# Optimization experiments

Measured on AMD Instinct MI355X. Metric: run time of the kernel, lower is better.

Reference implementation:

```python
import jax, jax.numpy as jnp
import numpy as np

B, S, D, H, F = 8, 1024, 768, 12, 3072
DH = D // H
C_QUAD = 5.0
LN_EPS = 1e-5


def layer_norm(x, g, b):
    mu = jnp.mean(x, axis=-1, keepdims=True)
    var = jnp.mean(jnp.square(x - mu), axis=-1, keepdims=True)
    return (x - mu) * jax.lax.rsqrt(var + LN_EPS) * g + b


def setup_inputs() -> dict:
    key = jax.random.key(0)
    ks = jax.random.split(key, 8)
    s_in = 1.0 / np.sqrt(D)
    s_ff = 1.0 / np.sqrt(F)
    return {
        "x": jax.random.normal(ks[0], (B, S, D), jnp.float32),
        "wqkv": jax.random.normal(ks[1], (D, 3 * D), jnp.float32) * s_in,
        "bqkv": jnp.zeros((3 * D,), jnp.float32),
        "wo": jax.random.normal(ks[2], (D, D), jnp.float32) * s_in,
        "bo": jnp.zeros((D,), jnp.float32),
        "ln1_g": jnp.ones((D,), jnp.float32),
        "ln1_b": jnp.zeros((D,), jnp.float32),
        "w1": jax.random.normal(ks[3], (D, F), jnp.float32) * s_in,
        "b1": jnp.zeros((F,), jnp.float32),
        "w2": jax.random.normal(ks[4], (F, D), jnp.float32) * s_ff,
        "b2": jnp.zeros((D,), jnp.float32),
        "ln2_g": jnp.ones((D,), jnp.float32),
        "ln2_b": jnp.zeros((D,), jnp.float32),
    }


def quad2(scores):
    # Quad2 custom 'softmax': (s + c)^2 normalized by row sum
    s2 = jnp.square(scores + C_QUAD)
    return s2 / jnp.sum(s2, axis=-1, keepdims=True)


def reference(x, wqkv, bqkv, wo, bo, ln1_g, ln1_b, w1, b1, w2, b2, ln2_g, ln2_b):
    # --- pre-norm multi-head attention with Quad2 score normalization ---
    h = layer_norm(x, ln1_g, ln1_b)
    qkv = h @ wqkv + bqkv                              # [B,S,3D]
    q, k, v = jnp.split(qkv, 3, axis=-1)
    q = q.reshape(B, S, H, DH).transpose(0, 2, 1, 3)   # [B,H,S,Dh]
    k = k.reshape(B, S, H, DH).transpose(0, 2, 1, 3)
    v = v.reshape(B, S, H, DH).transpose(0, 2, 1, 3)
    scale = 1.0 / np.sqrt(DH)
    scores = jnp.einsum("bhqd,bhkd->bhqk", q, k) * scale
    attn = quad2(scores)                               # [B,H,S,S]
    ctx = jnp.einsum("bhqk,bhkd->bhqd", attn, v)
    ctx = ctx.transpose(0, 2, 1, 3).reshape(B, S, D)
    x = x + ctx @ wo + bo
    # --- pre-norm FFN ---
    h = layer_norm(x, ln2_g, ln2_b)
    h = jax.nn.gelu(h @ w1 + b1)
    x = x + h @ w2 + b2
    return x
```

## Files before the change

kernel.cpp:

```cpp
#include <hip/hip_runtime.h>
#include <hip/hip_bf16.h>

constexpr int B_ = 8;
constexpr int S_ = 1024;
constexpr int D_ = 768;
constexpr int H_ = 12;
constexpr int F_ = 3072;
constexpr int DH_ = 64;
constexpr int M_ = B_ * S_;
constexpr int PSZ = B_ * S_ * D_;

typedef __bf16 bf16x8 __attribute__((ext_vector_type(8)));
typedef float f32x4 __attribute__((ext_vector_type(4)));
typedef short s16x8 __attribute__((ext_vector_type(8)));
typedef short s16x4 __attribute__((ext_vector_type(4)));

__device__ __forceinline__ void gload_lds16(const __bf16* g, __bf16* l) {
    __builtin_amdgcn_global_load_lds(
        (const __attribute__((address_space(1))) void*)g,
        (__attribute__((address_space(3))) void*)l,
        16, 0, 0);
}

__device__ __forceinline__ float fast_gelu(float x) {
    float z = 0.7978845608028654f * (x + 0.044715f * x * x * x);
    z = fminf(fmaxf(z, -15.0f), 15.0f);
    float e = __builtin_amdgcn_exp2f(2.8853900817779268f * z);
    float th = (e - 1.0f) / (e + 1.0f);
    return 0.5f * x * (1.0f + th);
}

__global__ __launch_bounds__(256) void transpose_cvt(const float* __restrict__ in,
                                                     __bf16* __restrict__ out,
                                                     int K, int N) {
    __shared__ float t[32][33];
    int tx = threadIdx.x, ty = threadIdx.y;
    int n0 = blockIdx.x * 32, k0 = blockIdx.y * 32;
#pragma unroll
    for (int i = 0; i < 4; ++i)
        t[ty + i * 8][tx] = in[(size_t)(k0 + ty + i * 8) * N + n0 + tx];
    __syncthreads();
#pragma unroll
    for (int i = 0; i < 4; ++i)
        out[(size_t)(n0 + ty + i * 8) * K + k0 + tx] = (__bf16)t[tx][ty + i * 8];
}

__global__ __launch_bounds__(256) void ln_kernel(const float* __restrict__ x,
                                                 const float* __restrict__ g,
                                                 const float* __restrict__ bb,
                                                 __bf16* __restrict__ out) {
    int row = blockIdx.x;
    const float* xr = x + (size_t)row * D_;
    int tid = threadIdx.x;
    float v[3];
    float s = 0.f, s2 = 0.f;
#pragma unroll
    for (int j = 0; j < 3; ++j) {
        v[j] = xr[tid + j * 256];
        s += v[j];
        s2 += v[j] * v[j];
    }
#pragma unroll
    for (int o = 32; o >= 1; o >>= 1) {
        s += __shfl_xor(s, o, 64);
        s2 += __shfl_xor(s2, o, 64);
    }
    __shared__ float red[8];
    int wid = tid >> 6, lane = tid & 63;
    if (lane == 0) { red[wid] = s; red[4 + wid] = s2; }
    __syncthreads();
    s = red[0] + red[1] + red[2] + red[3];
    s2 = red[4] + red[5] + red[6] + red[7];
    float mu = s * (1.0f / D_);
    float var = s2 * (1.0f / D_) - mu * mu;
    float rs = rsqrtf(var + 1e-5f);
    __bf16* orow = out + (size_t)row * D_;
#pragma unroll
    for (int j = 0; j < 3; ++j) {
        int i = tid + j * 256;
        orow[i] = (__bf16)((v[j] - mu) * rs * g[i] + bb[i]);
    }
}

template <int EPI>
__global__ __launch_bounds__(256) void gemm4(const __bf16* __restrict__ A,
                                             const __bf16* __restrict__ Bt,
                                             const float* __restrict__ bias,
                                             const float* __restrict__ res,
                                             float* __restrict__ outf,
                                             __bf16* __restrict__ outb,
                                             int M, int N, int K) {
    constexpr int BK = 64;
    __shared__ __bf16 lds[2][256 * BK];

    const int tid = threadIdx.x;
    const int lane = tid & 63, wid = tid >> 6;
    const int wm = wid >> 1, wn = wid & 1;
    const int bm = blockIdx.y * 128, bn = blockIdx.x * 128;
    const int l15 = lane & 15, l4 = lane >> 4;
    f32x4 acc[4][4] = {};

    const int r8 = tid >> 3;
    const int swc = ((tid & 7) ^ (r8 & 7)) * 8;
    const __bf16* ga = A + (size_t)(bm + r8) * K + swc;
    const __bf16* gb = Bt + (size_t)(bn + r8) * K + swc;
    const int NT = K / BK;

    auto stage = [&](int t, int s) {
        const int kt = t * BK;
        __bf16* base = &lds[s][0] + tid * 8;
#pragma unroll
        for (int j = 0; j < 4; ++j)
            gload_lds16(ga + kt + (size_t)j * 32 * K, base + j * 2048);
#pragma unroll
        for (int j = 0; j < 4; ++j)
            gload_lds16(gb + kt + (size_t)j * 32 * K, base + 8192 + j * 2048);
    };

    auto compute = [&](int s) {
        const __bf16* sA = &lds[s][0];
        const __bf16* sB = &lds[s][0] + 8192;
        const int swr = (l15 & 7) * 8;
        bf16x8 a[4][2], b[4][2];
#pragma unroll
        for (int mf = 0; mf < 4; ++mf) {
            int row = wm * 64 + mf * 16 + l15;
#pragma unroll
            for (int ks = 0; ks < 2; ++ks)
                a[mf][ks] = *(const bf16x8*)&sA[row * 64 + ((ks * 32 + l4 * 8) ^ swr)];
        }
#pragma unroll
        for (int nf = 0; nf < 4; ++nf) {
            int row = wn * 64 + nf * 16 + l15;
#pragma unroll
            for (int ks = 0; ks < 2; ++ks)
                b[nf][ks] = *(const bf16x8*)&sB[row * 64 + ((ks * 32 + l4 * 8) ^ swr)];
        }
        __builtin_amdgcn_s_setprio(1);
#pragma unroll
        for (int ks = 0; ks < 2; ++ks)
#pragma unroll
            for (int mf = 0; mf < 4; ++mf)
#pragma unroll
                for (int nf = 0; nf < 4; ++nf)
                    acc[mf][nf] = __builtin_amdgcn_mfma_f32_16x16x32_bf16(
                        a[mf][ks], b[nf][ks], acc[mf][nf], 0, 0, 0);
        __builtin_amdgcn_s_setprio(0);
    };

    stage(0, 0);
    for (int t = 0; t < NT; ++t) {
        if (t + 1 < NT) {
            stage(t + 1, (t + 1) & 1);
            asm volatile("s_waitcnt vmcnt(8)" ::: "memory");
        } else {
            asm volatile("s_waitcnt vmcnt(0)" ::: "memory");
        }
        asm volatile("s_barrier" ::: "memory");
        compute(t & 1);
        asm volatile("s_barrier" ::: "memory");
    }

#pragma unroll
    for (int mf = 0; mf < 4; ++mf) {
#pragma unroll
        for (int nf = 0; nf < 4; ++nf) {
#pragma unroll
            for (int r = 0; r < 4; ++r) {
                int m = bm + wm * 64 + mf * 16 + l4 * 4 + r;
                int n = bn + wn * 64 + nf * 16 + l15;
                float val = acc[mf][nf][r] + bias[n];
                if constexpr (EPI == 0) {
                    int part = n / 768;
                    int n7 = n - part * 768;
                    int head = n7 >> 6, dh = n7 & 63;
                    int bI = m >> 10, sI = m & 1023;
                    outb[(size_t)part * PSZ +
                         (((size_t)bI * H_ + head) * S_ + sI) * DH_ + dh] = (__bf16)val;
                } else if constexpr (EPI == 1) {
                    outf[(size_t)m * N + n] = val + res[(size_t)m * N + n];
                } else {
                    outb[(size_t)m * N + n] = (__bf16)fast_gelu(val);
                }
            }
        }
    }
}

__global__ __launch_bounds__(256) void attn_kernel(const __bf16* __restrict__ qg,
                                                   const __bf16* __restrict__ kg,
                                                   const __bf16* __restrict__ vg,
                                                   __bf16* __restrict__ ctx) {
    __shared__ __bf16 Ks[64][72];
    __shared__ __bf16 Vt[64][72];
    __shared__ __bf16 Pw[4][32][72];
    __shared__ float den_l[4][32];
    int tid = threadIdx.x, lane = tid & 63, wid = tid >> 6;
    int l15 = lane & 15, l4 = lane >> 4;
    int bh = blockIdx.x >> 3, qt = blockIdx.x & 7;
    int q0 = qt * 128;
    const __bf16* qbase = qg + (size_t)bh * S_ * DH_;
    const __bf16* kbase = kg + (size_t)bh * S_ * DH_;
    const __bf16* vbase = vg + (size_t)bh * S_ * DH_;

    int wq0 = q0 + wid * 32;
    bf16x8 qf[2][2];
#pragma unroll
    for (int qi = 0; qi < 2; ++qi)
#pragma unroll
        for (int ks = 0; ks < 2; ++ks)
            qf[qi][ks] = *(const bf16x8*)(qbase + (size_t)(wq0 + qi * 16 + l15) * DH_ +
                                          ks * 32 + l4 * 8);

    f32x4 oacc[2][4] = {};
    float den[2] = {0.f, 0.f};
    const float scale = 0.125f;

    for (int k0 = 0; k0 < S_; k0 += 64) {
        {
            int key = tid >> 2, dc = (tid & 3) * 16;
            *(s16x8*)&Ks[key][dc] =
                *(const s16x8*)(kbase + (size_t)(k0 + key) * DH_ + dc);
            *(s16x8*)&Ks[key][dc + 8] =
                *(const s16x8*)(kbase + (size_t)(k0 + key) * DH_ + dc + 8);
            int vkey = tid & 63, dg = (tid >> 6) * 16;
            s16x8 v0 = *(const s16x8*)(vbase + (size_t)(k0 + vkey) * DH_ + dg);
            s16x8 v1 = *(const s16x8*)(vbase + (size_t)(k0 + vkey) * DH_ + dg + 8);
#pragma unroll
            for (int e = 0; e < 8; ++e) {
                Vt[dg + e][vkey] = ((const __bf16*)&v0)[e];
                Vt[dg + 8 + e][vkey] = ((const __bf16*)&v1)[e];
            }
        }
        __syncthreads();

        bf16x8 kf[4][2];
#pragma unroll
        for (int kfi = 0; kfi < 4; ++kfi)
#pragma unroll
            for (int ks = 0; ks < 2; ++ks)
                kf[kfi][ks] = *(const bf16x8*)&Ks[kfi * 16 + l15][ks * 32 + l4 * 8];

#pragma unroll
        for (int qi = 0; qi < 2; ++qi) {
#pragma unroll
            for (int kfi = 0; kfi < 4; ++kfi) {
                f32x4 sa = {};
                sa = __builtin_amdgcn_mfma_f32_16x16x32_bf16(kf[kfi][0], qf[qi][0], sa, 0, 0, 0);
                sa = __builtin_amdgcn_mfma_f32_16x16x32_bf16(kf[kfi][1], qf[qi][1], sa, 0, 0, 0);
                __bf16 pk[4];
#pragma unroll
                for (int r = 0; r < 4; ++r) {
                    float p = sa[r] * scale + 5.0f;
                    p = p * p;
                    den[qi] += p;
                    pk[r] = (__bf16)p;
                }
                *(s16x4*)&Pw[wid][qi * 16 + l15][kfi * 16 + l4 * 4] =
                    *(const s16x4*)pk;
            }
        }

#pragma unroll
        for (int mf = 0; mf < 2; ++mf) {
#pragma unroll
            for (int ks = 0; ks < 2; ++ks) {
                bf16x8 pa = *(const bf16x8*)&Pw[wid][mf * 16 + l15][ks * 32 + l4 * 8];
#pragma unroll
                for (int nf = 0; nf < 4; ++nf) {
                    bf16x8 vb = *(const bf16x8*)&Vt[nf * 16 + l15][ks * 32 + l4 * 8];
                    oacc[mf][nf] = __builtin_amdgcn_mfma_f32_16x16x32_bf16(
                        pa, vb, oacc[mf][nf], 0, 0, 0);
                }
            }
        }
        __syncthreads();
    }

#pragma unroll
    for (int qi = 0; qi < 2; ++qi) {
        den[qi] += __shfl_xor(den[qi], 16, 64);
        den[qi] += __shfl_xor(den[qi], 32, 64);
    }
    if (lane < 16) {
        den_l[wid][lane] = den[0];
        den_l[wid][16 + lane] = den[1];
    }
    __syncthreads();

    int b_ = bh / H_, h_ = bh - b_ * H_;
#pragma unroll
    for (int mf = 0; mf < 2; ++mf)
#pragma unroll
        for (int nf = 0; nf < 4; ++nf)
#pragma unroll
            for (int r = 0; r < 4; ++r) {
                int qrow = mf * 16 + l4 * 4 + r;
                int dcol = nf * 16 + l15;
                float val = oacc[mf][nf][r] / den_l[wid][qrow];
                int sI = q0 + wid * 32 + qrow;
                ctx[((size_t)b_ * S_ + sI) * D_ + h_ * DH_ + dcol] = (__bf16)val;
            }
}

extern "C" void kernel_launch(void* const* d_in, const int* in_sizes, int n_in,
                              void* d_out, int out_size, void* d_ws, size_t ws_size,
                              hipStream_t stream) {
    const float* x    = (const float*)d_in[0];
    const float* wqkv = (const float*)d_in[1];
    const float* bqkv = (const float*)d_in[2];
    const float* wo   = (const float*)d_in[3];
    const float* bo   = (const float*)d_in[4];
    const float* ln1g = (const float*)d_in[5];
    const float* ln1b = (const float*)d_in[6];
    const float* w1   = (const float*)d_in[7];
    const float* b1   = (const float*)d_in[8];
    const float* w2   = (const float*)d_in[9];
    const float* b2   = (const float*)d_in[10];
    const float* ln2g = (const float*)d_in[11];
    const float* ln2b = (const float*)d_in[12];
    float* out = (float*)d_out;

    char* ws = (char*)d_ws;
    size_t off = 0;
    auto alloc = [&](size_t bytes) {
        void* p = ws + off;
        off += (bytes + 255) & ~(size_t)255;
        return p;
    };
    __bf16* wqkvT = (__bf16*)alloc((size_t)(3 * D_) * D_ * 2);
    __bf16* woT   = (__bf16*)alloc((size_t)D_ * D_ * 2);
    __bf16* w1T   = (__bf16*)alloc((size_t)F_ * D_ * 2);
    __bf16* w2T   = (__bf16*)alloc((size_t)D_ * F_ * 2);
    float*  X2    = (float*)alloc((size_t)M_ * D_ * 4);
    __bf16* Hb    = (__bf16*)alloc((size_t)M_ * D_ * 2);
    __bf16* Q3    = (__bf16*)alloc((size_t)4 * PSZ * 2);
    __bf16* Kb = Q3 + (size_t)PSZ;
    __bf16* Vb = Q3 + (size_t)2 * PSZ;
    __bf16* Cx = Q3 + (size_t)3 * PSZ;

    transpose_cvt<<<dim3((3 * D_) / 32, D_ / 32), dim3(32, 8), 0, stream>>>(wqkv, wqkvT, D_, 3 * D_);
    transpose_cvt<<<dim3(D_ / 32, D_ / 32), dim3(32, 8), 0, stream>>>(wo, woT, D_, D_);
    transpose_cvt<<<dim3(F_ / 32, D_ / 32), dim3(32, 8), 0, stream>>>(w1, w1T, D_, F_);
    transpose_cvt<<<dim3(D_ / 32, F_ / 32), dim3(32, 8), 0, stream>>>(w2, w2T, F_, D_);

    ln_kernel<<<M_, 256, 0, stream>>>(x, ln1g, ln1b, Hb);
    gemm4<0><<<dim3((3 * D_) / 128, M_ / 128), 256, 0, stream>>>(
        Hb, wqkvT, bqkv, nullptr, nullptr, Q3, M_, 3 * D_, D_);
    attn_kernel<<<B_ * H_ * (S_ / 128), 256, 0, stream>>>(Q3, Kb, Vb, Cx);
    gemm4<1><<<dim3(D_ / 128, M_ / 128), 256, 0, stream>>>(
        Cx, woT, bo, x, X2, nullptr, M_, D_, D_);
    ln_kernel<<<M_, 256, 0, stream>>>(X2, ln2g, ln2b, Hb);
    gemm4<2><<<dim3(F_ / 128, M_ / 128), 256, 0, stream>>>(
        Hb, w1T, b1, nullptr, nullptr, Q3, M_, F_, D_);
    gemm4<1><<<dim3(D_ / 128, M_ / 128), 256, 0, stream>>>(
        Q3, w2T, b2, X2, out, nullptr, M_, D_, F_);
    (void)in_sizes; (void)n_in; (void)out_size; (void)ws_size;
}
```

Baseline: 255.3 us.

## Remap GEMM workgroups across XCDs, restructure K loop and epilogues, use fast reciprocals

Several independent changes land together. GEMM workgroup IDs are permuted so consecutive tiles spread across the 8 XCDs for better L2 locality. The LDS reads are now followed by an lgkmcnt wait and a barrier before the MFMAs, which releases the LDS buffer earlier. The QKV epilogue hoists address arithmetic out of the inner loop. GELU becomes a sigmoid form using rcp, and the attention normalization multiplies by rcp instead of dividing. These trade small precision differences and an extra barrier for less ALU work, with some risk that the XCD remap ordering is not exact when the grid is not divisible by 8.

```diff
diff --git a/kernel.cpp b/kernel.cpp
--- a/kernel.cpp
+++ b/kernel.cpp
@@ -23,11 +23,10 @@
 }
 
 __device__ __forceinline__ float fast_gelu(float x) {
-    float z = 0.7978845608028654f * (x + 0.044715f * x * x * x);
-    z = fminf(fmaxf(z, -15.0f), 15.0f);
-    float e = __builtin_amdgcn_exp2f(2.8853900817779268f * z);
-    float th = (e - 1.0f) / (e + 1.0f);
-    return 0.5f * x * (1.0f + th);
+    float x3 = x * x * x;
+    float z = 0.7978845608028654f * x + 0.035677408136300125f * x3;
+    float e = __builtin_amdgcn_exp2f(-2.8853900817779268f * z);
+    return x * __builtin_amdgcn_rcpf(1.0f + e);
 }
 
 __global__ __launch_bounds__(256) void transpose_cvt(const float* __restrict__ in,
@@ -96,7 +95,11 @@
     const int tid = threadIdx.x;
     const int lane = tid & 63, wid = tid >> 6;
     const int wm = wid >> 1, wn = wid & 1;
-    const int bm = blockIdx.y * 128, bn = blockIdx.x * 128;
+    const int gx = gridDim.x;
+    const int nwg = gx * gridDim.y;
+    int flat = blockIdx.y * gx + blockIdx.x;
+    flat = (flat & 7) * (nwg >> 3) + (flat >> 3);
+    const int bm = (flat / gx) * 128, bn = (flat % gx) * 128;
     const int l15 = lane & 15, l4 = lane >> 4;
     f32x4 acc[4][4] = {};
 
@@ -115,37 +118,6 @@
 #pragma unroll
         for (int j = 0; j < 4; ++j)
             gload_lds16(gb + kt + (size_t)j * 32 * K, base + 8192 + j * 2048);
-    };
-
-    auto compute = [&](int s) {
-        const __bf16* sA = &lds[s][0];
-        const __bf16* sB = &lds[s][0] + 8192;
-        const int swr = (l15 & 7) * 8;
-        bf16x8 a[4][2], b[4][2];
-#pragma unroll
-        for (int mf = 0; mf < 4; ++mf) {
-            int row = wm * 64 + mf * 16 + l15;
-#pragma unroll
-            for (int ks = 0; ks < 2; ++ks)
-                a[mf][ks] = *(const bf16x8*)&sA[row * 64 + ((ks * 32 + l4 * 8) ^ swr)];
-        }
-#pragma unroll
-        for (int nf = 0; nf < 4; ++nf) {
-            int row = wn * 64 + nf * 16 + l15;
-#pragma unroll
-            for (int ks = 0; ks < 2; ++ks)
-                b[nf][ks] = *(const bf16x8*)&sB[row * 64 + ((ks * 32 + l4 * 8) ^ swr)];
-        }
-        __builtin_amdgcn_s_setprio(1);
-#pragma unroll
-        for (int ks = 0; ks < 2; ++ks)
-#pragma unroll
-            for (int mf = 0; mf < 4; ++mf)
-#pragma unroll
-                for (int nf = 0; nf < 4; ++nf)
-                    acc[mf][nf] = __builtin_amdgcn_mfma_f32_16x16x32_bf16(
-                        a[mf][ks], b[nf][ks], acc[mf][nf], 0, 0, 0);
-        __builtin_amdgcn_s_setprio(0);
     };
 
     stage(0, 0);
@@ -157,30 +129,74 @@
             asm volatile("s_waitcnt vmcnt(0)" ::: "memory");
         }
         asm volatile("s_barrier" ::: "memory");
-        compute(t & 1);
+
+        const __bf16* sA = &lds[t & 1][0];
+        const __bf16* sB = sA + 8192;
+        const int swr = (l15 & 7) * 8;
+        bf16x8 a[4][2], b[4][2];
+#pragma unroll
+        for (int mf = 0; mf < 4; ++mf) {
+            int row = wm * 64 + mf * 16 + l15;
+#pragma unroll
+            for (int ks = 0; ks < 2; ++ks)
+                a[mf][ks] = *(const bf16x8*)&sA[row * 64 + ((ks * 32 + l4 * 8) ^ swr)];
+        }
+#pragma unroll
+        for (int nf = 0; nf < 4; ++nf) {
+            int row = wn * 64 + nf * 16 + l15;
+#pragma unroll
+            for (int ks = 0; ks < 2; ++ks)
+                b[nf][ks] = *(const bf16x8*)&sB[row * 64 + ((ks * 32 + l4 * 8) ^ swr)];
+        }
+        asm volatile("s_waitcnt lgkmcnt(0)" ::: "memory");
         asm volatile("s_barrier" ::: "memory");
-    }
-
-#pragma unroll
-    for (int mf = 0; mf < 4; ++mf) {
+        __builtin_amdgcn_sched_barrier(0);
+
+        __builtin_amdgcn_s_setprio(1);
+#pragma unroll
+        for (int ks = 0; ks < 2; ++ks)
+#pragma unroll
+            for (int mf = 0; mf < 4; ++mf)
+#pragma unroll
+                for (int nf = 0; nf < 4; ++nf)
+                    acc[mf][nf] = __builtin_amdgcn_mfma_f32_16x16x32_bf16(
+                        a[mf][ks], b[nf][ks], acc[mf][nf], 0, 0, 0);
+        __builtin_amdgcn_s_setprio(0);
+    }
+
+    if constexpr (EPI == 0) {
 #pragma unroll
         for (int nf = 0; nf < 4; ++nf) {
-#pragma unroll
-            for (int r = 0; r < 4; ++r) {
-                int m = bm + wm * 64 + mf * 16 + l4 * 4 + r;
-                int n = bn + wn * 64 + nf * 16 + l15;
-                float val = acc[mf][nf][r] + bias[n];
-                if constexpr (EPI == 0) {
-                    int part = n / 768;
-                    int n7 = n - part * 768;
-                    int head = n7 >> 6, dh = n7 & 63;
-                    int bI = m >> 10, sI = m & 1023;
-                    outb[(size_t)part * PSZ +
-                         (((size_t)bI * H_ + head) * S_ + sI) * DH_ + dh] = (__bf16)val;
-                } else if constexpr (EPI == 1) {
-                    outf[(size_t)m * N + n] = val + res[(size_t)m * N + n];
-                } else {
-                    outb[(size_t)m * N + n] = (__bf16)fast_gelu(val);
+            int n = bn + wn * 64 + nf * 16 + l15;
+            int part = n / 768;
+            int n7 = n - part * 768;
+            float bv = bias[n];
+            size_t obase = (size_t)part * PSZ + (size_t)(n7 >> 6) * (S_ * DH_) + (n7 & 63);
+#pragma unroll
+            for (int mf = 0; mf < 4; ++mf) {
+                int m0 = bm + wm * 64 + mf * 16 + l4 * 4;
+                size_t rb = obase + (size_t)(m0 >> 10) * ((size_t)H_ * S_ * DH_) +
+                            (size_t)(m0 & 1023) * DH_;
+#pragma unroll
+                for (int r = 0; r < 4; ++r)
+                    outb[rb + (size_t)r * DH_] = (__bf16)(acc[mf][nf][r] + bv);
+            }
+        }
+    } else {
+#pragma unroll
+        for (int mf = 0; mf < 4; ++mf) {
+#pragma unroll
+            for (int nf = 0; nf < 4; ++nf) {
+#pragma unroll
+                for (int r = 0; r < 4; ++r) {
+                    int m = bm + wm * 64 + mf * 16 + l4 * 4 + r;
+                    int n = bn + wn * 64 + nf * 16 + l15;
+                    float val = acc[mf][nf][r] + bias[n];
+                    if constexpr (EPI == 1) {
+                        outf[(size_t)m * N + n] = val + res[(size_t)m * N + n];
+                    } else {
+                        outb[(size_t)m * N + n] = (__bf16)fast_gelu(val);
+                    }
                 }
             }
         }
@@ -292,15 +308,17 @@
 #pragma unroll
     for (int mf = 0; mf < 2; ++mf)
 #pragma unroll
-        for (int nf = 0; nf < 4; ++nf)
+        for (int nf = 0; nf < 4; ++nf) {
 #pragma unroll
             for (int r = 0; r < 4; ++r) {
                 int qrow = mf * 16 + l4 * 4 + r;
                 int dcol = nf * 16 + l15;
-                float val = oacc[mf][nf][r] / den_l[wid][qrow];
+                float val = oacc[mf][nf][r] *
+                            __builtin_amdgcn_rcpf(den_l[wid][qrow]);
                 int sI = q0 + wid * 32 + qrow;
                 ctx[((size_t)b_ * S_ + sI) * D_ + h_ * DH_ + dcol] = (__bf16)val;
             }
+        }
 }
 
 extern "C" void kernel_launch(void* const* d_in, const int* in_sizes, int n_in,
```

After: 219.7 us. 1.16x faster.
